# Performance work log

Hardware: AMD Instinct MI355X
Metric: run time of the kernel (lower is better)

## Reference

```python
import jax, jax.numpy as jnp
import numpy as np

NUM, K = 5, 3
IN_DIM, D_OUT = 512, 512
N_U, BATCH, GATED_IN = 64, 8192, 576
NB = NUM + K + 1  # 9 basis channels (num+k splines + 1 SiLU base)
TERM_SIZES = (4, 8)
TERM_MULTS = (32768, 16384)  # 4*32768 + 8*16384 = 262144 = D_OUT*IN_DIM
WDIM = 128


def extend_grid(grid, k):
    # grid: (S, num+1) -> (S, num+1+2k), appending k knots each side with uniform spacing h
    h = (grid[:, -1:] - grid[:, :1]) / (grid.shape[1] - 1)
    left = grid[:, :1] + h * jnp.arange(-k, 0, dtype=grid.dtype)
    right = grid[:, -1:] + h * jnp.arange(1, k + 1, dtype=grid.dtype)
    return jnp.concatenate([left, grid, right], axis=1)


def B_batch(x, grid, k):
    # Cox-de-Boor recursion. x: (S, B), grid: (S, G) extended. Returns (S, G-k-1, B).
    xg = x[:, None, :]
    g = grid[:, :, None]
    v = ((xg >= g[:, :-1]) & (xg < g[:, 1:])).astype(x.dtype)
    for p in range(1, k + 1):
        v = (xg - g[:, :-(p + 1)]) / (g[:, p:-1] - g[:, :-(p + 1)]) * v[:, :-1] \
          + (g[:, p + 1:] - xg) / (g[:, p + 1:] - g[:, 1:-p]) * v[:, 1:]
    return v


def lazy_P(terms, mults, perm, w):
    # emlp-style lazy equivariant projector: permute rows, apply small block
    # projectors with multiplicities, un-permute. w: (R, C).
    invperm = jnp.argsort(perm)
    wp = w[perm]
    outs, off = [], 0
    for P, m in zip(terms, mults):
        s = P.shape[0]
        blk = wp[off:off + m * s].reshape(m, s, -1)
        outs.append(jnp.einsum('ij,mjc->mic', P, blk).reshape(m * s, -1))
        off += m * s
    return jnp.concatenate(outs, axis=0)[invperm]


def setup_inputs() -> dict:
    key = jax.random.key(0)
    ks = jax.random.split(key, 12)
    x = jax.random.normal(ks[0], (BATCH, GATED_IN), dtype=jnp.float32)
    grid = jnp.tile(jnp.linspace(-1.0, 1.0, NUM + 1, dtype=jnp.float32)[None, :], (N_U, 1))
    linear_weight = 0.05 * jax.random.normal(ks[1], (D_OUT, NB * IN_DIM), dtype=jnp.float32)
    linear_bias = 0.05 * jax.random.normal(ks[2], (D_OUT,), dtype=jnp.float32)
    P_term_a = 0.3 * jax.random.normal(ks[3], (TERM_SIZES[0], TERM_SIZES[0]), dtype=jnp.float32)
    P_term_b = 0.3 * jax.random.normal(ks[4], (TERM_SIZES[1], TERM_SIZES[1]), dtype=jnp.float32)
    Pb = (1.0 / np.sqrt(D_OUT)) * jax.random.normal(ks[5], (D_OUT, D_OUT), dtype=jnp.float32)
    bi_basis = 0.01 * jax.random.normal(ks[6], (WDIM, D_OUT, D_OUT), dtype=jnp.float32)
    bi_w = jax.random.normal(ks[7], (WDIM,), dtype=jnp.float32)
    u = jnp.sort(jax.random.randint(ks[8], (N_U,), 0, GATED_IN))
    indices = jax.random.randint(ks[9], (IN_DIM,), 0, N_U)
    perm = jax.random.permutation(ks[10], D_OUT * IN_DIM)
    return {"x": x, "grid": grid, "linear_weight": linear_weight, "linear_bias": linear_bias,
            "P_term_a": P_term_a, "P_term_b": P_term_b, "Pb": Pb,
            "bi_basis": bi_basis, "bi_w": bi_w, "u": u, "indices": indices, "perm": perm}


def reference(x, grid, linear_weight, linear_bias, P_term_a, P_term_b, Pb, bi_basis, bi_w, u, indices, perm):
    batch = x.shape[0]
    # gather gate scalars and build spline + base activations
    gs = x[:, u].T                                   # (S, B)
    eg = extend_grid(grid, K)                        # (S, num+1+2k)
    sp = B_batch(gs, eg, K)                          # (S, num+k, B)
    sp = jnp.transpose(sp, (2, 1, 0))                # (B, num+k, S)
    sb = jax.nn.silu(gs).T[:, None, :]               # (B, 1, S)
    g = jnp.concatenate([sp, sb], axis=1)            # (B, NB, S)
    g = g[:, :, indices]                             # (B, NB, in_dim) gather via inverse indices
    acts = (g * x[:, None, :IN_DIM]).reshape(batch, -1)  # (B, NB*in_dim)
    # equivariant weight projection
    w_r = linear_weight.reshape(D_OUT, NB, IN_DIM).transpose(0, 2, 1).reshape(D_OUT * IN_DIM, NB)
    W_r = lazy_P([P_term_a, P_term_b], TERM_MULTS, perm, w_r)
    W = W_r.reshape(D_OUT, IN_DIM, NB).transpose(0, 2, 1).reshape(D_OUT, NB * IN_DIM)
    b = Pb @ linear_bias
    out = acts @ W.T + b                             # (B, D_OUT)
    # bilinear equivariant mix
    bi_W = jnp.einsum('w,wij->ij', bi_w, bi_basis)   # (D_OUT, D_OUT)
    out = 0.1 * (out @ bi_W.T) + out
    return out
```

## Files before the change

kernel.cpp:

```cpp
#include <hip/hip_runtime.h>

#define DI __device__ __forceinline__

typedef __attribute__((ext_vector_type(8))) short short8;
typedef __attribute__((ext_vector_type(4))) float f32x4;

DI ushort f2bf(float f) {
  union { float f; unsigned u; } v; v.f = f;
  unsigned r = v.u + 0x7fffu + ((v.u >> 16) & 1u);
  return (ushort)(r >> 16);
}

DI void gload_lds16(const void* g, void* l) {
  __builtin_amdgcn_global_load_lds((const __attribute__((address_space(1))) void*)g,
                                   (__attribute__((address_space(3))) void*)l, 16, 0, 0);
}


__global__ __launch_bounds__(256) void k_biW(const float2* __restrict__ bb,
                                             const float* __restrict__ bw,
                                             float2* __restrict__ Mf32,
                                             uint* __restrict__ Mbf16) {
  __shared__ float w[128];
  int tid = threadIdx.x;
  if (tid < 128) w[tid] = bw[tid];
  __syncthreads();
  int t = blockIdx.x * 256 + tid;
  const float2* p = bb + t;
  float ax = 0.f, ay = 0.f;
#pragma unroll 16
  for (int k = 0; k < 128; ++k) {
    float2 v = p[(size_t)k * 131072];
    float s = w[k];
    ax += s * v.x; ay += s * v.y;
  }
  int i = t >> 8, j0 = (t & 255) * 2;
  float2 r;
  r.x = 0.1f * ax + (i == j0 + 0 ? 1.f : 0.f);
  r.y = 0.1f * ay + (i == j0 + 1 ? 1.f : 0.f);
  Mf32[t] = r;
  Mbf16[t] = (uint)f2bf(r.x) | ((uint)f2bf(r.y) << 16);
}

__global__ __launch_bounds__(256) void k_matvec(const float* __restrict__ A,
                                                const float* __restrict__ v,
                                                float* __restrict__ y) {
  int o = blockIdx.x * 4 + (threadIdx.x >> 6);
  int lane = threadIdx.x & 63;
  float acc = 0.f;
  for (int k = lane; k < 512; k += 64) acc += A[o * 512 + k] * v[k];
#pragma unroll
  for (int s = 32; s; s >>= 1) acc += __shfl_down(acc, s, 64);
  if (lane == 0) y[o] = acc;
}

__global__ __launch_bounds__(256) void k_lazyP(const float* __restrict__ LW,
                                               const float* __restrict__ Pa,
                                               const float* __restrict__ Pb8,
                                               const int* __restrict__ perm,
                                               ushort* __restrict__ Wt) {
  int q = blockIdx.x * 256 + threadIdx.x;
  int lane = threadIdx.x & 63;
  int r = perm[q];
  int o = r >> 9, ic = r & 511;
  int a_own = o * 4608 + ic;
  if (q < 131072) {
    int ii = lane & 3, g = lane & ~3;
    float pp[4];
#pragma unroll
    for (int j = 0; j < 4; ++j) pp[j] = Pa[ii * 4 + j];
#pragma unroll
    for (int c = 0; c < 9; ++c) {
      float v = LW[a_own + c * 512];
      float acc = 0.f;
#pragma unroll
      for (int j = 0; j < 4; ++j) acc += pp[j] * __shfl(v, g + j, 64);
      Wt[(size_t)(c * 512 + ic) * 512 + o] = f2bf(acc);
    }
  } else {
    int ii = lane & 7, g = lane & ~7;
    float pp[8];
#pragma unroll
    for (int j = 0; j < 8; ++j) pp[j] = Pb8[ii * 8 + j];
#pragma unroll
    for (int c = 0; c < 9; ++c) {
      float v = LW[a_own + c * 512];
      float acc = 0.f;
#pragma unroll
      for (int j = 0; j < 8; ++j) acc += pp[j] * __shfl(v, g + j, 64);
      Wt[(size_t)(c * 512 + ic) * 512 + o] = f2bf(acc);
    }
  }
}

__global__ __launch_bounds__(256) void k_acts(const float* __restrict__ x,
                                              const float* __restrict__ grid,
                                              const int* __restrict__ u,
                                              const int* __restrict__ indices,
                                              ushort* __restrict__ acts) {
  __shared__ float basis[8][64][9];
  __shared__ int sidx[512];
  int tid = threadIdx.x;
  int b0 = blockIdx.x * 8;
  for (int i = tid; i < 512; i += 256) sidx[i] = indices[i];
#pragma unroll
  for (int e0 = 0; e0 < 2; ++e0) {
    int e = e0 * 256 + tid;
    int row = e >> 6, j = e & 63;
    float gs = x[(size_t)(b0 + row) * 576 + u[j]];
    float g0 = grid[j * 6], g5 = grid[j * 6 + 5];
    float h = (g5 - g0) * 0.2f;
    float lo = g0 - 3.f * h;
    float tt = (gs - lo) / h;
#pragma unroll
    for (int n = 0; n < 8; ++n) basis[row][j][n] = 0.f;
    float fc = floorf(tt);
    int c = (int)fc;
    if (c >= 0 && c <= 10) {
      float t = tt - fc;
      float t2 = t * t, t3 = t2 * t;
      float om = 1.f - t;
      float w0 = t3 * (1.f / 6.f);
      float w1 = (1.f + 3.f * t + 3.f * t2 - 3.f * t3) * (1.f / 6.f);
      float w2 = (4.f - 6.f * t2 + 3.f * t3) * (1.f / 6.f);
      float w3 = om * om * om * (1.f / 6.f);
      if (c <= 7) basis[row][j][c] = w0;
      if (c >= 1 && c <= 8) basis[row][j][c - 1] = w1;
      if (c >= 2 && c <= 9) basis[row][j][c - 2] = w2;
      if (c >= 3) basis[row][j][c - 3] = w3;
    }
    basis[row][j][8] = gs / (1.f + __expf(-gs));
  }
  __syncthreads();
#pragma unroll
  for (int rep = 0; rep < 2; ++rep) {
    int e = rep * 256 + tid;
    int row = e >> 6, i0 = (e & 63) * 8;
    size_t xb = (size_t)(b0 + row) * 576;
    float4 xa = *(const float4*)&x[xb + i0];
    float4 xc = *(const float4*)&x[xb + i0 + 4];
    int4 ja = *(const int4*)&sidx[i0];
    int4 jb = *(const int4*)&sidx[i0 + 4];
    size_t ab = (size_t)(b0 + row) * 4608 + i0;
#pragma unroll
    for (int n = 0; n < 9; ++n) {
      short8 hv;
      hv[0] = (short)f2bf(basis[row][ja.x][n] * xa.x);
      hv[1] = (short)f2bf(basis[row][ja.y][n] * xa.y);
      hv[2] = (short)f2bf(basis[row][ja.z][n] * xa.z);
      hv[3] = (short)f2bf(basis[row][ja.w][n] * xa.w);
      hv[4] = (short)f2bf(basis[row][jb.x][n] * xc.x);
      hv[5] = (short)f2bf(basis[row][jb.y][n] * xc.y);
      hv[6] = (short)f2bf(basis[row][jb.z][n] * xc.z);
      hv[7] = (short)f2bf(basis[row][jb.w][n] * xc.w);
      *(short8*)(&acts[ab + (size_t)n * 512]) = hv;
    }
  }
}

template <int BM, int BN>
__global__ __launch_bounds__(256) void gemm_bt(const ushort* __restrict__ A,
                                               const ushort* __restrict__ B,
                                               ushort* __restrict__ Cout,
                                               int N, int Kd) {
  constexpr int BK = 64;
  constexpr int FM = BM / 32;
  constexpr int FN = BN / 32;
  __shared__ __align__(16) ushort Al[2][BM * BK];
  __shared__ __align__(16) ushort Bl[2][BN * BK];
  int tid = threadIdx.x, lane = tid & 63, wid = tid >> 6;
  int wm = wid >> 1, wn = wid & 1;
  int tiles_n = N / BN;
  int per_xcd = gridDim.x >> 3;
  int flat = (blockIdx.x & 7) * per_xcd + (blockIdx.x >> 3);
  int bm = flat / tiles_n, bn = flat % tiles_n;
  long m0 = (long)bm * BM;
  long n0 = (long)bn * BN;
  int swc = ((tid & 7) ^ ((tid >> 3) & 7)) * 8;
  const ushort* agp = A + (m0 + (tid >> 3)) * (long)Kd + swc;
  const ushort* bgp = B + (n0 + (tid >> 3)) * (long)Kd + swc;

#define STAGE64(buf, k0)                                                      \
  do {                                                                        \
    _Pragma("unroll")                                                         \
    for (int it = 0; it < BM / 32; ++it)                                      \
      gload_lds16(agp + (it * 32) * (long)Kd + (k0), &Al[buf][(it * 256 + tid) * 8]); \
    _Pragma("unroll")                                                         \
    for (int it = 0; it < BN / 32; ++it)                                      \
      gload_lds16(bgp + (it * 32) * (long)Kd + (k0), &Bl[buf][(it * 256 + tid) * 8]); \
  } while (0)

  f32x4 acc[FM][FN] = {};
  int swz = (lane & 7) << 3;
  int nt = Kd / BK;
  STAGE64(0, 0);
  __syncthreads();
  for (int t = 0; t < nt; ++t) {
    int cur = t & 1;
    if (t + 1 < nt) STAGE64(cur ^ 1, (t + 1) * BK);
#pragma unroll
    for (int ks = 0; ks < 2; ++ks) {
      int kidx = (ks * 32 + (lane >> 4) * 8) ^ swz;
      short8 a[FM], b[FN];
#pragma unroll
      for (int f = 0; f < FM; ++f)
        a[f] = *(const short8*)&Al[cur][(wm * (FM * 16) + f * 16 + (lane & 15)) * BK + kidx];
#pragma unroll
      for (int f = 0; f < FN; ++f)
        b[f] = *(const short8*)&Bl[cur][(wn * (FN * 16) + f * 16 + (lane & 15)) * BK + kidx];
#pragma unroll
      for (int i = 0; i < FM; ++i)
#pragma unroll
        for (int j = 0; j < FN; ++j)
          acc[i][j] = __builtin_amdgcn_mfma_f32_16x16x32_bf16(a[i], b[j], acc[i][j], 0, 0, 0);
    }
    __syncthreads();
  }
#undef STAGE64
#pragma unroll
  for (int i = 0; i < FM; ++i)
#pragma unroll
    for (int j = 0; j < FN; ++j) {
      int row_b = wm * (FM * 16) + i * 16 + ((lane >> 4) * 4);
      long col = n0 + wn * (FN * 16) + j * 16 + (lane & 15);
#pragma unroll
      for (int r = 0; r < 4; ++r)
        Cout[(m0 + row_b + r) * N + col] = f2bf(acc[i][j][r]);
    }
}

__global__ __launch_bounds__(256, 2) void gemm_sk(const ushort* __restrict__ A,
                                                  const ushort* __restrict__ B,
                                                  const float* __restrict__ b2,
                                                  float* __restrict__ P0,
                                                  float* __restrict__ P1) {
  constexpr int BM = 128, BN = 128, BK = 64, FM = 4, FN = 4;
  const int Kd = 4608, N = 512;
  __shared__ __align__(16) ushort Al[2][BM * BK];
  __shared__ __align__(16) ushort Bl[2][BN * BK];
  int tid = threadIdx.x, lane = tid & 63, wid = tid >> 6;
  int wm = wid >> 1, wn = wid & 1;
  int flat = (blockIdx.x & 7) * 64 + (blockIdx.x >> 3);
  int bm = flat >> 3, kb = (flat >> 2) & 1, bn = flat & 3;
  long m0 = (long)bm * BM, n0 = (long)bn * BN;
  int kbase = kb * 2304;
  float* Pout = kb ? P1 : P0;

  int swc = ((tid & 7) ^ ((tid >> 3) & 7)) * 8;
  const ushort* agp = A + (m0 + (tid >> 3)) * (long)Kd + kbase + swc;
  const ushort* bgp = B + (n0 + (tid >> 3)) * (long)Kd + kbase + swc;

#define STAGE(buf, k0)                                                        \
  do {                                                                        \
    _Pragma("unroll")                                                         \
    for (int it = 0; it < 4; ++it)                                            \
      gload_lds16(agp + (it * 32) * (long)Kd + (k0), &Al[buf][(it * 256 + tid) * 8]); \
    _Pragma("unroll")                                                         \
    for (int it = 0; it < 4; ++it)                                            \
      gload_lds16(bgp + (it * 32) * (long)Kd + (k0), &Bl[buf][(it * 256 + tid) * 8]); \
  } while (0)

  f32x4 acc[FM][FN] = {};
  int swz = (lane & 7) << 3;
  const int nt = 2304 / BK;
  STAGE(0, 0);
  __syncthreads();
  for (int t = 0; t < nt; ++t) {
    int cur = t & 1;
    if (t + 1 < nt) STAGE(cur ^ 1, (t + 1) * BK);
#pragma unroll
    for (int ks = 0; ks < 2; ++ks) {
      int kidx = (ks * 32 + (lane >> 4) * 8) ^ swz;
      short8 a[FM], b[FN];
#pragma unroll
      for (int f = 0; f < FM; ++f)
        a[f] = *(const short8*)&Al[cur][(wm * 64 + f * 16 + (lane & 15)) * BK + kidx];
#pragma unroll
      for (int f = 0; f < FN; ++f)
        b[f] = *(const short8*)&Bl[cur][(wn * 64 + f * 16 + (lane & 15)) * BK + kidx];
#pragma unroll
      for (int i = 0; i < FM; ++i)
#pragma unroll
        for (int j = 0; j < FN; ++j)
          acc[i][j] = __builtin_amdgcn_mfma_f32_16x16x32_bf16(a[i], b[j], acc[i][j], 0, 0, 0);
    }
    __syncthreads();
  }
#undef STAGE
#pragma unroll
  for (int i = 0; i < FM; ++i)
#pragma unroll
    for (int j = 0; j < FN; ++j) {
      int row_b = wm * 64 + i * 16 + ((lane >> 4) * 4);
      long col = n0 + wn * 64 + j * 16 + (lane & 15);
      float bv = (kb == 0) ? b2[col] : 0.f;
#pragma unroll
      for (int r = 0; r < 4; ++r)
        Pout[(m0 + row_b + r) * N + col] = acc[i][j][r] + bv;
    }
}

__global__ __launch_bounds__(256) void k_reduce(float4* __restrict__ P0,
                                                const float4* __restrict__ P1) {
  int t = blockIdx.x * 256 + threadIdx.x;
#pragma unroll
  for (int rep = 0; rep < 2; ++rep) {
    int e = rep * 524288 + t;
    float4 a = P0[e], b = P1[e];
    a.x += b.x; a.y += b.y; a.z += b.z; a.w += b.w;
    P0[e] = a;
  }
}

extern "C" void kernel_launch(void* const* d_in, const int* in_sizes, int n_in,
                              void* d_out, int out_size, void* d_ws, size_t ws_size,
                              hipStream_t stream) {
  const float* x        = (const float*)d_in[0];
  const float* grid     = (const float*)d_in[1];
  const float* LW       = (const float*)d_in[2];
  const float* lb       = (const float*)d_in[3];
  const float* Pa       = (const float*)d_in[4];
  const float* Pb8      = (const float*)d_in[5];
  const float* Pbm      = (const float*)d_in[6];
  const float* bi_basis = (const float*)d_in[7];
  const float* bi_w     = (const float*)d_in[8];
  const int*   u        = (const int*)d_in[9];
  const int*   indices  = (const int*)d_in[10];
  const int*   perm     = (const int*)d_in[11];
  float* out = (float*)d_out;
  char* ws = (char*)d_ws;

  float*  Mf32  = (float*)(ws + 0);
  ushort* Mbf16 = (ushort*)(ws + 1048576);
  float*  tvec  = (float*)(ws + 1572864);
  float*  b2    = (float*)(ws + 1576960);
  ushort* Wt    = (ushort*)(ws + 2097152);
  ushort* W2    = (ushort*)(ws + 6815744);
  ushort* acts  = (ushort*)(ws + 11534336);
  float*  P1    = (float*)(ws + 87031808);

  k_biW<<<512, 256, 0, stream>>>((const float2*)bi_basis, bi_w, (float2*)Mf32, (uint*)Mbf16);
  k_matvec<<<128, 256, 0, stream>>>(Pbm, lb, tvec);
  k_matvec<<<128, 256, 0, stream>>>(Mf32, tvec, b2);
  k_lazyP<<<1024, 256, 0, stream>>>(LW, Pa, Pb8, perm, Wt);
  gemm_bt<64, 128><<<(512 / 64) * (4608 / 128), 256, 0, stream>>>(
      Mbf16, Wt, W2, 4608, 512);
  k_acts<<<1024, 256, 0, stream>>>(x, grid, u, indices, acts);
  gemm_sk<<<512, 256, 0, stream>>>(acts, W2, b2, out, P1);
  k_reduce<<<2048, 256, 0, stream>>>((float4*)out, (const float4*)P1);
}
```

Before: 167.6 us.

## Split lazy projector into mix, inverse-permutation and coalesced gather kernels

The single lazy-projection kernel, which scattered 2-byte bf16 writes to a transposed layout, is replaced by three kernels. One builds a transposed inverse permutation, one writes the mixed weights contiguously in permuted order, and one gathers them into the transposed layout with 16-byte vector stores. The aim is to turn uncoalesced scattered writes into coalesced writes plus gathered reads. In exchange it adds two kernel launches, an extra intermediate buffer round trip, and random 2-byte reads in the gather.

```diff
diff --git a/kernel.cpp b/kernel.cpp
--- a/kernel.cpp
+++ b/kernel.cpp
@@ -54,11 +54,18 @@
   if (lane == 0) y[o] = acc;
 }
 
-__global__ __launch_bounds__(256) void k_lazyP(const float* __restrict__ LW,
-                                               const float* __restrict__ Pa,
-                                               const float* __restrict__ Pb8,
-                                               const int* __restrict__ perm,
-                                               ushort* __restrict__ Wt) {
+__global__ __launch_bounds__(256) void k_invp(const int* __restrict__ perm,
+                                              int* __restrict__ invT) {
+  int q = blockIdx.x * 256 + threadIdx.x;
+  int r = perm[q];
+  invT[(r & 511) * 512 + (r >> 9)] = q;
+}
+
+__global__ __launch_bounds__(256) void k_mix(const float* __restrict__ LW,
+                                             const float* __restrict__ Pa,
+                                             const float* __restrict__ Pb8,
+                                             const int* __restrict__ perm,
+                                             ushort* __restrict__ Wmix) {
   int q = blockIdx.x * 256 + threadIdx.x;
   int lane = threadIdx.x & 63;
   int r = perm[q];
@@ -75,7 +82,7 @@
       float acc = 0.f;
 #pragma unroll
       for (int j = 0; j < 4; ++j) acc += pp[j] * __shfl(v, g + j, 64);
-      Wt[(size_t)(c * 512 + ic) * 512 + o] = f2bf(acc);
+      Wmix[c * 262144 + q] = f2bf(acc);
     }
   } else {
     int ii = lane & 7, g = lane & ~7;
@@ -88,9 +95,29 @@
       float acc = 0.f;
 #pragma unroll
       for (int j = 0; j < 8; ++j) acc += pp[j] * __shfl(v, g + j, 64);
-      Wt[(size_t)(c * 512 + ic) * 512 + o] = f2bf(acc);
-    }
-  }
+      Wmix[c * 262144 + q] = f2bf(acc);
+    }
+  }
+}
+
+__global__ __launch_bounds__(256) void k_gather(const int* __restrict__ invT,
+                                                const ushort* __restrict__ Wmix,
+                                                ushort* __restrict__ Wt) {
+  int gid = blockIdx.x * 256 + threadIdx.x;
+  int L = gid * 8;
+  int c = L >> 18;
+  int ic = (L >> 9) & 511;
+  int o0 = L & 511;
+  const int* ip = &invT[ic * 512 + o0];
+  int4 qa = *(const int4*)ip;
+  int4 qb = *(const int4*)(ip + 4);
+  const ushort* wm = &Wmix[c * 262144];
+  short8 v;
+  v[0] = (short)wm[qa.x]; v[1] = (short)wm[qa.y];
+  v[2] = (short)wm[qa.z]; v[3] = (short)wm[qa.w];
+  v[4] = (short)wm[qb.x]; v[5] = (short)wm[qb.y];
+  v[6] = (short)wm[qb.z]; v[7] = (short)wm[qb.w];
+  *(short8*)&Wt[L] = v;
 }
 
 __global__ __launch_bounds__(256) void k_acts(const float* __restrict__ x,
@@ -338,11 +365,15 @@
   ushort* W2    = (ushort*)(ws + 6815744);
   ushort* acts  = (ushort*)(ws + 11534336);
   float*  P1    = (float*)(ws + 87031808);
+  int*    invT  = (int*)(ws + 103809024);
+  ushort* Wmix  = (ushort*)(ws + 104857600);
 
   k_biW<<<512, 256, 0, stream>>>((const float2*)bi_basis, bi_w, (float2*)Mf32, (uint*)Mbf16);
   k_matvec<<<128, 256, 0, stream>>>(Pbm, lb, tvec);
   k_matvec<<<128, 256, 0, stream>>>(Mf32, tvec, b2);
-  k_lazyP<<<1024, 256, 0, stream>>>(LW, Pa, Pb8, perm, Wt);
+  k_invp<<<1024, 256, 0, stream>>>(perm, invT);
+  k_mix<<<1024, 256, 0, stream>>>(LW, Pa, Pb8, perm, Wmix);
+  k_gather<<<1152, 256, 0, stream>>>(invT, Wmix, Wt);
   gemm_bt<64, 128><<<(512 / 64) * (4608 / 128), 256, 0, stream>>>(
       Mbf16, Wt, W2, 4608, 512);
   k_acts<<<1024, 256, 0, stream>>>(x, grid, u, indices, acts);
```

New measurement: 158.9 us. 5.2% less time.
